# Kernel tuning notes

Hardware: AMD Instinct MI355X
Metric: run time of the kernel (lower is better)

## Reference

```python
import jax, jax.numpy as jnp
import numpy as np


def setup_inputs() -> dict:
    key = jax.random.key(0)
    k1, k2 = jax.random.split(key)
    B, N, M, D = 16, 2048, 2048, 3
    predictions = jax.random.normal(k1, (B, N, D), dtype=jnp.float32)
    targets = jax.random.normal(k2, (B, M, D), dtype=jnp.float32)
    return {"predictions": predictions, "targets": targets}


def reference(predictions, targets):
    # Batched pairwise squared distances: [B, N, M]
    # d(i,j) = |x_i|^2 + |y_j|^2 - 2 x_i . y_j
    xx = jnp.sum(predictions * predictions, axis=-1)  # [B, N]
    yy = jnp.sum(targets * targets, axis=-1)          # [B, M]
    xy = jnp.einsum("bnd,bmd->bnm", predictions, targets)  # [B, N, M]
    P = xx[:, :, None] + yy[:, None, :] - 2.0 * xy    # [B, N, M]
    # Chamfer: sum of per-point nearest-neighbor squared distances, both directions
    loss = jnp.sum(jnp.min(P, axis=2)) + jnp.sum(jnp.min(P, axis=1))
    return loss
```

## Files before the change

### kernel.cpp

```cpp
#include <hip/hip_runtime.h>
#include <math.h>


typedef float v2f __attribute__((ext_vector_type(2)));

#define NPTS    2048
#define NCOMBO  32
#define KSLICE  16
#define SLICE   128
#define SPT     8

__device__ __forceinline__ v2f pkfma(v2f a, v2f b, v2f c) {
#if __has_builtin(__builtin_elementwise_fma)
    return __builtin_elementwise_fma(a, b, c);
#else
    v2f d; d.x = fmaf(a.x, b.x, c.x); d.y = fmaf(a.y, b.y, c.y); return d;
#endif
}

__global__ __launch_bounds__(256, 2) void chamfer_partial(
    const float* __restrict__ preds,
    const float* __restrict__ tgts,
    float* __restrict__ partial,
    float* __restrict__ out)
{
    __shared__ __align__(16) float qx[SLICE];
    __shared__ __align__(16) float qy[SLICE];
    __shared__ __align__(16) float qz[SLICE];
    __shared__ __align__(16) float qw[SLICE];

    const int bid   = blockIdx.x;
    const int combo = bid & (NCOMBO - 1);
    const int slice = bid >> 5;
    const int dir   = combo >> 4;
    const int b     = combo & 15;

    if (bid == 0 && threadIdx.x == 0) out[0] = 0.0f;

    const float* src = (dir ? tgts : preds) + (size_t)b * NPTS * 3;
    const float* opp = (dir ? preds : tgts) + (size_t)b * NPTS * 3;

    if (threadIdx.x < SLICE) {
        const int jj = slice * SLICE + threadIdx.x;
        const float y0 = opp[3 * jj + 0];
        const float y1 = opp[3 * jj + 1];
        const float y2 = opp[3 * jj + 2];
        qx[threadIdx.x] = y0;
        qy[threadIdx.x] = y1;
        qz[threadIdx.x] = y2;
        qw[threadIdx.x] = y0 * y0 + y1 * y1 + y2 * y2;
    }

    v2f nn0[SPT], nn1[SPT], nn2[SPT];
    float m[SPT];
    #pragma unroll
    for (int k = 0; k < SPT; k++) {
        const int i = threadIdx.x + 256 * k;
        const float a0 = -2.0f * src[3 * i + 0];
        const float a1 = -2.0f * src[3 * i + 1];
        const float a2 = -2.0f * src[3 * i + 2];
        nn0[k] = (v2f){a0, a0};
        nn1[k] = (v2f){a1, a1};
        nn2[k] = (v2f){a2, a2};
        m[k]   = INFINITY;
    }
    __syncthreads();

    #pragma unroll 2
    for (int jg = 0; jg < SLICE / 4; jg++) {
        const float4 X = *(const float4*)&qx[4 * jg];
        const float4 Y = *(const float4*)&qy[4 * jg];
        const float4 Z = *(const float4*)&qz[4 * jg];
        const float4 W = *(const float4*)&qw[4 * jg];
        const v2f Xa = {X.x, X.y}, Xb = {X.z, X.w};
        const v2f Ya = {Y.x, Y.y}, Yb = {Y.z, Y.w};
        const v2f Za = {Z.x, Z.y}, Zb = {Z.z, Z.w};
        const v2f Wa = {W.x, W.y}, Wb = {W.z, W.w};
        #pragma unroll
        for (int k = 0; k < SPT; k++) {
            const v2f sa = pkfma(nn0[k], Xa, pkfma(nn1[k], Ya, pkfma(nn2[k], Za, Wa)));
            m[k] = fminf(fminf(m[k], sa.x), sa.y);
            const v2f sb = pkfma(nn0[k], Xb, pkfma(nn1[k], Yb, pkfma(nn2[k], Zb, Wb)));
            m[k] = fminf(fminf(m[k], sb.x), sb.y);
        }
    }

    float* pp = partial + ((size_t)combo * KSLICE + slice) * NPTS;
    #pragma unroll
    for (int k = 0; k < SPT; k++)
        pp[threadIdx.x + 256 * k] = m[k];
}

__global__ __launch_bounds__(256) void chamfer_reduce(
    const float* __restrict__ preds,
    const float* __restrict__ tgts,
    const float* __restrict__ partial,
    float* __restrict__ out)
{
    __shared__ float wsum[4];

    const int idx   = blockIdx.x * 256 + threadIdx.x;
    const int combo = idx >> 11;
    const int i     = idx & (NPTS - 1);
    const int dir   = combo >> 4;
    const int b     = combo & 15;

    const float* src = (dir ? tgts : preds) + (size_t)b * NPTS * 3;
    const float x0 = src[3 * i + 0];
    const float x1 = src[3 * i + 1];
    const float x2 = src[3 * i + 2];
    const float xx = x0 * x0 + x1 * x1 + x2 * x2;

    const float* pp = partial + (size_t)combo * KSLICE * NPTS + i;
    float mn = pp[0];
    #pragma unroll
    for (int s = 1; s < KSLICE; s++)
        mn = fminf(mn, pp[(size_t)s * NPTS]);

    float val = xx + mn;

    #pragma unroll
    for (int off = 32; off > 0; off >>= 1)
        val += __shfl_down(val, off, 64);

    const int lane = threadIdx.x & 63;
    const int wid  = threadIdx.x >> 6;
    if (lane == 0) wsum[wid] = val;
    __syncthreads();
    if (threadIdx.x == 0)
        atomicAdd(out, wsum[0] + wsum[1] + wsum[2] + wsum[3]);
}

extern "C" void kernel_launch(void* const* d_in, const int* in_sizes, int n_in,
                              void* d_out, int out_size, void* d_ws, size_t ws_size,
                              hipStream_t stream) {
    const float* preds = (const float*)d_in[0];
    const float* tgts  = (const float*)d_in[1];
    float* out     = (float*)d_out;
    float* partial = (float*)d_ws;

    chamfer_partial<<<NCOMBO * KSLICE, 256, 0, stream>>>(preds, tgts, partial, out);
    chamfer_reduce<<<(2 * 16 * NPTS) / 256, 256, 0, stream>>>(preds, tgts, partial, out);
}
```

Before: 71.12 us.

## Retile chamfer partial kernel: wider target slices, fewer points per thread, vector loads

Each block now handles half of the source points (4 contiguous points per thread) against a 256-point target slice, so there are 8 slices instead of 16 and twice as many blocks. Source points are read with three float4 loads per thread and partial minima are written with a single float4 store. The aim is to halve the partial buffer the reduce kernel must read, coalesce the global accesses, and use the full block for the shared-memory fill. The trade-off is lower per-thread register reuse of each shared-memory target load, since each target is now applied to 4 points instead of 8.

```diff
diff --git a/kernel.cpp b/kernel.cpp
--- a/kernel.cpp
+++ b/kernel.cpp
@@ -6,9 +6,9 @@
 
 #define NPTS    2048
 #define NCOMBO  32
-#define KSLICE  16
-#define SLICE   128
-#define SPT     8
+#define KSLICE  8
+#define SLICE   256
+#define SPT     4
 
 __device__ __forceinline__ v2f pkfma(v2f a, v2f b, v2f c) {
 #if __has_builtin(__builtin_elementwise_fma)
@@ -31,7 +31,9 @@
 
     const int bid   = blockIdx.x;
     const int combo = bid & (NCOMBO - 1);
-    const int slice = bid >> 5;
+    const int rest  = bid >> 5;
+    const int slice = rest >> 1;
+    const int half  = rest & 1;
     const int dir   = combo >> 4;
     const int b     = combo & 15;
 
@@ -40,7 +42,7 @@
     const float* src = (dir ? tgts : preds) + (size_t)b * NPTS * 3;
     const float* opp = (dir ? preds : tgts) + (size_t)b * NPTS * 3;
 
-    if (threadIdx.x < SLICE) {
+    {
         const int jj = slice * SLICE + threadIdx.x;
         const float y0 = opp[3 * jj + 0];
         const float y1 = opp[3 * jj + 1];
@@ -51,22 +53,32 @@
         qw[threadIdx.x] = y0 * y0 + y1 * y1 + y2 * y2;
     }
 
+    const int i0 = half * 1024 + SPT * threadIdx.x;
+    const float4 r0 = *(const float4*)&src[3 * i0 + 0];
+    const float4 r1 = *(const float4*)&src[3 * i0 + 4];
+    const float4 r2 = *(const float4*)&src[3 * i0 + 8];
     v2f nn0[SPT], nn1[SPT], nn2[SPT];
+    {
+        const float px[SPT] = {r0.x, r0.w, r1.z, r2.y};
+        const float py[SPT] = {r0.y, r1.x, r1.w, r2.z};
+        const float pz[SPT] = {r0.z, r1.y, r2.x, r2.w};
+        #pragma unroll
+        for (int k = 0; k < SPT; k++) {
+            const float a0 = -2.0f * px[k];
+            const float a1 = -2.0f * py[k];
+            const float a2 = -2.0f * pz[k];
+            nn0[k] = (v2f){a0, a0};
+            nn1[k] = (v2f){a1, a1};
+            nn2[k] = (v2f){a2, a2};
+        }
+    }
     float m[SPT];
     #pragma unroll
-    for (int k = 0; k < SPT; k++) {
-        const int i = threadIdx.x + 256 * k;
-        const float a0 = -2.0f * src[3 * i + 0];
-        const float a1 = -2.0f * src[3 * i + 1];
-        const float a2 = -2.0f * src[3 * i + 2];
-        nn0[k] = (v2f){a0, a0};
-        nn1[k] = (v2f){a1, a1};
-        nn2[k] = (v2f){a2, a2};
-        m[k]   = INFINITY;
-    }
+    for (int k = 0; k < SPT; k++) m[k] = INFINITY;
+
     __syncthreads();
 
-    #pragma unroll 2
+    #pragma unroll 4
     for (int jg = 0; jg < SLICE / 4; jg++) {
         const float4 X = *(const float4*)&qx[4 * jg];
         const float4 Y = *(const float4*)&qy[4 * jg];
@@ -85,10 +97,8 @@
         }
     }
 
-    float* pp = partial + ((size_t)combo * KSLICE + slice) * NPTS;
-    #pragma unroll
-    for (int k = 0; k < SPT; k++)
-        pp[threadIdx.x + 256 * k] = m[k];
+    float* pp = partial + ((size_t)combo * KSLICE + slice) * NPTS + i0;
+    *(float4*)pp = make_float4(m[0], m[1], m[2], m[3]);
 }
 
 __global__ __launch_bounds__(256) void chamfer_reduce(
@@ -139,6 +149,6 @@
     float* out     = (float*)d_out;
     float* partial = (float*)d_ws;
 
-    chamfer_partial<<<NCOMBO * KSLICE, 256, 0, stream>>>(preds, tgts, partial, out);
+    chamfer_partial<<<NCOMBO * KSLICE * 2, 256, 0, stream>>>(preds, tgts, partial, out);
     chamfer_reduce<<<(2 * 16 * NPTS) / 256, 256, 0, stream>>>(preds, tgts, partial, out);
 }
```

Measured after the change: 71.21 us. About the same (+0.1%).
